# Performance work log

Measured on AMD Instinct MI355X. Metric: run time of the kernel, lower is better.

Reference implementation:

```python
import jax, jax.numpy as jnp
import numpy as np

D, H, KVH, HD, FF = 768, 12, 4, 64, 2048
N_REP = H // KVH
EPS = 1e-6


def rmsnorm(x, w):
    # Faithful to source: norm = ||x|| * n^{-1/2}; eps added to norm (not inside sqrt)
    norm = jnp.sqrt(jnp.sum(x * x, axis=-1, keepdims=True)) * (x.shape[-1] ** -0.5)
    return w * x / (norm + EPS)


def rope_tables(seq_len, head_dim, base=10000.0):
    inv_freq = 1.0 / (base ** (np.arange(0, head_dim, 2, dtype=np.float32) / head_dim))
    t = np.arange(seq_len, dtype=np.float32)
    freqs = np.einsum('i,j->ij', t, inv_freq)  # [S, HD/2]
    emb = np.concatenate([freqs, freqs], axis=-1)  # [S, HD]
    return jnp.asarray(np.cos(emb)), jnp.asarray(np.sin(emb))


def rotate_half(x):
    h = x.shape[-1] // 2
    return jnp.concatenate([-x[..., h:], x[..., :h]], axis=-1)


def setup_inputs() -> dict:
    key = jax.random.key(0)
    ks = jax.random.split(key, 9)
    s = 0.02
    return {
        'x': jax.random.normal(ks[0], (2, 2048, D), jnp.float32),
        'Wq': jax.random.normal(ks[1], (H * HD, D), jnp.float32) * s,
        'Wk': jax.random.normal(ks[2], (KVH * HD, D), jnp.float32) * s,
        'Wv': jax.random.normal(ks[3], (KVH * HD, D), jnp.float32) * s,
        'Wo': jax.random.normal(ks[4], (D, H * HD), jnp.float32) * s,
        'Wgate': jax.random.normal(ks[5], (FF, D), jnp.float32) * s,
        'Wup': jax.random.normal(ks[6], (FF, D), jnp.float32) * s,
        'Wdown': jax.random.normal(ks[7], (D, FF), jnp.float32) * s,
        'g1': jnp.ones((D,), jnp.float32),
        'g2': jnp.ones((D,), jnp.float32),
    }


def reference(x, Wq, Wk, Wv, Wo, Wgate, Wup, Wdown, g1, g2):
    B, S, _ = x.shape
    # ---- attention sublayer (pre-norm) ----
    xn = rmsnorm(x, g1)
    q = (xn @ Wq.T).reshape(B, S, H, HD).transpose(0, 2, 1, 3)      # [B,H,S,HD]
    k = (xn @ Wk.T).reshape(B, S, KVH, HD).transpose(0, 2, 1, 3)    # [B,KVH,S,HD]
    v = (xn @ Wv.T).reshape(B, S, KVH, HD).transpose(0, 2, 1, 3)
    cos, sin = rope_tables(S, HD)                                   # [S,HD]
    q = q * cos + rotate_half(q) * sin
    k = k * cos + rotate_half(k) * sin
    # repeat kv heads to match q heads
    k = jnp.repeat(k, N_REP, axis=1)                                # [B,H,S,HD]
    v = jnp.repeat(v, N_REP, axis=1)
    scores = jnp.einsum('bhqd,bhkd->bhqk', q, k) / jnp.sqrt(jnp.float32(HD))
    causal = jnp.tril(jnp.ones((S, S), bool))
    scores = jnp.where(causal, scores, jnp.finfo(scores.dtype).min)
    attn = jax.nn.softmax(scores, axis=-1)
    out = jnp.einsum('bhqk,bhkd->bhqd', attn, v)                    # [B,H,S,HD]
    out = out.transpose(0, 2, 1, 3).reshape(B, S, H * HD) @ Wo.T
    x = x + out
    # ---- SwiGLU FFN sublayer (pre-norm) ----
    xn2 = rmsnorm(x, g2)
    ff = (jax.nn.silu(xn2 @ Wgate.T) * (xn2 @ Wup.T)) @ Wdown.T
    return x + ff
```

## Files before the change

### kernel.cpp

```cpp
#include <hip/hip_runtime.h>
#include <hip/hip_bf16.h>
#include <math.h>

typedef __bf16 bf16;
typedef __attribute__((ext_vector_type(8))) __bf16 bf16x8;
typedef __attribute__((ext_vector_type(4))) __bf16 bf16x4;
typedef __attribute__((ext_vector_type(4))) float f32x4;

#define MFMA16(a,b,c) __builtin_amdgcn_mfma_f32_16x16x32_bf16(a,b,c,0,0,0)

#define BATCH 2
#define SEQ   2048
#define DMODEL 768
#define NH    12
#define NKV   4
#define NREP  3
#define HD    64
#define FFDIM 2048
#define ROWS  (BATCH*SEQ)

#define QSCALE 0.18033688011112042f
#define LOG2E  1.4426950408889634f

__device__ __forceinline__ void gl2lds16(const bf16* g, bf16* l) {
  __builtin_amdgcn_global_load_lds(
      (const __attribute__((address_space(1))) void*)g,
      (__attribute__((address_space(3))) void*)l, 16, 0, 0);
}

__device__ __forceinline__ bf16x8 pack8(f32x4 a, f32x4 b) {
  bf16x8 o;
  o[0] = (bf16)a[0]; o[1] = (bf16)a[1]; o[2] = (bf16)a[2]; o[3] = (bf16)a[3];
  o[4] = (bf16)b[0]; o[5] = (bf16)b[1]; o[6] = (bf16)b[2]; o[7] = (bf16)b[3];
  return o;
}

__global__ __launch_bounds__(256) void rope_tab_kernel(float* __restrict__ tab) {
  int id = blockIdx.x * 256 + threadIdx.x;
  int j = id >> 11, s = id & 2047;
  float inv = expf(-(float)j * (9.210340371976184f / 32.0f));
  float ang = (float)s * inv;
  tab[id] = cosf(ang);
  tab[65536 + id] = sinf(ang);
}

__global__ __launch_bounds__(256) void rmsnorm_kernel(const float* __restrict__ x,
    const float* __restrict__ g, bf16* __restrict__ out) {
  int row = blockIdx.x;
  const float* xr = x + (size_t)row * DMODEL;
  int t = threadIdx.x;
  float v0 = xr[t], v1 = xr[t + 256], v2 = xr[t + 512];
  float ss = v0 * v0 + v1 * v1 + v2 * v2;
  #pragma unroll
  for (int off = 32; off; off >>= 1) ss += __shfl_xor(ss, off, 64);
  __shared__ float red[4];
  if ((t & 63) == 0) red[t >> 6] = ss;
  __syncthreads();
  float total = red[0] + red[1] + red[2] + red[3];
  float norm = sqrtf(total) * 0.03608439182435161f;
  float sc = 1.0f / (norm + 1e-6f);
  bf16* orow = out + (size_t)row * DMODEL;
  orow[t]       = (bf16)(g[t]       * v0 * sc);
  orow[t + 256] = (bf16)(g[t + 256] * v1 * sc);
  orow[t + 512] = (bf16)(g[t + 512] * v2 * sc);
}

template<bool RES, typename OUTT>
__global__ __launch_bounds__(256) void gemm_bt64f_kernel(const bf16* __restrict__ A,
    const float* __restrict__ Bf, OUTT* __restrict__ C, const float* __restrict__ R,
    int N, int K) {
  __shared__ __align__(16) bf16 At[64 * 32];
  __shared__ __align__(16) bf16 Bt[128 * 32];
  int t = threadIdx.x;
  int lane = t & 63;
  int wave = t >> 6;
  int l15 = lane & 15, lq = lane >> 4;
  int wrow = (wave >> 1) * 32, wcol = (wave & 1) * 64;
  int row0 = blockIdx.y * 64;
  int col0 = blockIdx.x * 128;
  int srow = t >> 2, sseg = (t & 3) * 8;
  const bf16* Ag0 = A + (size_t)(row0 + srow) * K + sseg;
  const float* Bg0 = Bf + (size_t)(col0 + srow) * K + sseg;
  const float* Bg1 = Bg0 + (size_t)64 * K;
  bf16* Al0 = At + t * 8;
  bf16* Bl0 = Bt + t * 8;
  bf16* Bl1 = Bt + 2048 + t * 8;

  f32x4 b0a = *(const f32x4*)(Bg0), b0b = *(const f32x4*)(Bg0 + 4);
  f32x4 b1a = *(const f32x4*)(Bg1), b1b = *(const f32x4*)(Bg1 + 4);

  f32x4 zero = {0.f, 0.f, 0.f, 0.f};
  f32x4 acc[2][4];
  #pragma unroll
  for (int m = 0; m < 2; ++m)
    #pragma unroll
    for (int n = 0; n < 4; ++n) acc[m][n] = zero;

  for (int k0 = 0; k0 < K; k0 += 32) {
    __syncthreads();
    gl2lds16(Ag0 + k0, Al0);
    *(bf16x8*)Bl0 = pack8(b0a, b0b);
    *(bf16x8*)Bl1 = pack8(b1a, b1b);
    if (k0 + 32 < K) {
      b0a = *(const f32x4*)(Bg0 + k0 + 32); b0b = *(const f32x4*)(Bg0 + k0 + 36);
      b1a = *(const f32x4*)(Bg1 + k0 + 32); b1b = *(const f32x4*)(Bg1 + k0 + 36);
    }
    __syncthreads();
    bf16x8 af[2], bfr[4];
    #pragma unroll
    for (int m = 0; m < 2; ++m)
      af[m] = *(const bf16x8*)(At + (wrow + m * 16 + l15) * 32 + lq * 8);
    #pragma unroll
    for (int n = 0; n < 4; ++n)
      bfr[n] = *(const bf16x8*)(Bt + (wcol + n * 16 + l15) * 32 + lq * 8);
    #pragma unroll
    for (int m = 0; m < 2; ++m)
      #pragma unroll
      for (int n = 0; n < 4; ++n)
        acc[m][n] = MFMA16(af[m], bfr[n], acc[m][n]);
  }
  #pragma unroll
  for (int m = 0; m < 2; ++m)
    #pragma unroll
    for (int n = 0; n < 4; ++n)
      #pragma unroll
      for (int r = 0; r < 4; ++r) {
        size_t idx = (size_t)(row0 + wrow + m * 16 + lq * 4 + r) * N
                   + (col0 + wcol + n * 16 + l15);
        float v = acc[m][n][r];
        if (RES) v += R[idx];
        C[idx] = (OUTT)v;
      }
}

__global__ __launch_bounds__(256) void gemm_qkv_kernel(const bf16* __restrict__ A,
    const float* __restrict__ Wq, const float* __restrict__ Wk, const float* __restrict__ Wv,
    const float* __restrict__ tab, bf16* __restrict__ Qh, bf16* __restrict__ Kh,
    bf16* __restrict__ Vt) {
  __shared__ __align__(16) bf16 At[64 * 32];
  __shared__ __align__(16) bf16 Bt[128 * 32];
  const int K = DMODEL;
  int t = threadIdx.x;
  int lane = t & 63, wave = t >> 6;
  int l15 = lane & 15, lq = lane >> 4;
  int wrow = (wave >> 1) * 32, wcol = (wave & 1) * 64;
  int row0 = blockIdx.y * 64;
  int col0 = blockIdx.x * 128;
  int srow = t >> 2, sseg = (t & 3) * 8;

  const float* Bsrc; int brow;
  if (col0 < 768)       { Bsrc = Wq; brow = col0; }
  else if (col0 < 1024) { Bsrc = Wk; brow = col0 - 768; }
  else                  { Bsrc = Wv; brow = col0 - 1024; }

  const bf16* Ag0 = A + (size_t)(row0 + srow) * K + sseg;
  const float* Bg0 = Bsrc + (size_t)(brow + srow) * K + sseg;
  const float* Bg1 = Bg0 + (size_t)64 * K;
  bf16* Al0 = At + t * 8;
  bf16* Bl0 = Bt + t * 8;
  bf16* Bl1 = Bt + 2048 + t * 8;

  f32x4 b0a = *(const f32x4*)(Bg0), b0b = *(const f32x4*)(Bg0 + 4);
  f32x4 b1a = *(const f32x4*)(Bg1), b1b = *(const f32x4*)(Bg1 + 4);

  f32x4 zero = {0.f, 0.f, 0.f, 0.f};
  f32x4 acc[2][4];
  #pragma unroll
  for (int m = 0; m < 2; ++m)
    #pragma unroll
    for (int n = 0; n < 4; ++n) acc[m][n] = zero;

  for (int k0 = 0; k0 < K; k0 += 32) {
    __syncthreads();
    gl2lds16(Ag0 + k0, Al0);
    *(bf16x8*)Bl0 = pack8(b0a, b0b);
    *(bf16x8*)Bl1 = pack8(b1a, b1b);
    if (k0 + 32 < K) {
      b0a = *(const f32x4*)(Bg0 + k0 + 32); b0b = *(const f32x4*)(Bg0 + k0 + 36);
      b1a = *(const f32x4*)(Bg1 + k0 + 32); b1b = *(const f32x4*)(Bg1 + k0 + 36);
    }
    __syncthreads();
    bf16x8 af[2], bfr[4];
    #pragma unroll
    for (int m = 0; m < 2; ++m)
      af[m] = *(const bf16x8*)(At + (wrow + m * 16 + l15) * 32 + lq * 8);
    #pragma unroll
    for (int n = 0; n < 4; ++n)
      bfr[n] = *(const bf16x8*)(Bt + (wcol + n * 16 + l15) * 32 + lq * 8);
    #pragma unroll
    for (int m = 0; m < 2; ++m)
      #pragma unroll
      for (int n = 0; n < 4; ++n)
        acc[m][n] = MFMA16(af[m], bfr[n], acc[m][n]);
  }

  int b = row0 >> 11;
  int s0 = (row0 & 2047) + wrow + lq * 4;
  int colw = col0 + wcol;
  if (colw < 768) {
    int h = colw >> 6;
    f32x4 cv[2][2], sv[2][2];
    #pragma unroll
    for (int m = 0; m < 2; ++m)
      #pragma unroll
      for (int jh = 0; jh < 2; ++jh) {
        const float* cp = tab + (jh * 16 + l15) * 2048 + s0 + m * 16;
        cv[m][jh] = *(const f32x4*)cp;
        sv[m][jh] = *(const f32x4*)(cp + 65536);
      }
    #pragma unroll
    for (int m = 0; m < 2; ++m)
      #pragma unroll
      for (int n = 0; n < 4; ++n) {
        float sgn = (n < 2) ? -1.f : 1.f;
        #pragma unroll
        for (int r = 0; r < 4; ++r) {
          float c = cv[m][n & 1][r], si = sv[m][n & 1][r];
          float rp = (acc[m][n][r] * c + sgn * acc[m][n ^ 2][r] * si) * QSCALE;
          Qh[((size_t)(b * NH + h) * SEQ + s0 + m * 16 + r) * 64 + n * 16 + l15] = (bf16)rp;
        }
      }
  } else if (colw < 1024) {
    int kh = (colw - 768) >> 6;
    f32x4 cv[2][2], sv[2][2];
    #pragma unroll
    for (int m = 0; m < 2; ++m)
      #pragma unroll
      for (int jh = 0; jh < 2; ++jh) {
        const float* cp = tab + (jh * 16 + l15) * 2048 + s0 + m * 16;
        cv[m][jh] = *(const f32x4*)cp;
        sv[m][jh] = *(const f32x4*)(cp + 65536);
      }
    #pragma unroll
    for (int m = 0; m < 2; ++m)
      #pragma unroll
      for (int n = 0; n < 4; ++n) {
        float sgn = (n < 2) ? -1.f : 1.f;
        #pragma unroll
        for (int r = 0; r < 4; ++r) {
          float c = cv[m][n & 1][r], si = sv[m][n & 1][r];
          float rp = acc[m][n][r] * c + sgn * acc[m][n ^ 2][r] * si;
          Kh[((size_t)(b * NKV + kh) * SEQ + s0 + m * 16 + r) * 64 + n * 16 + l15] = (bf16)rp;
        }
      }
  } else {
    int vh = (colw - 1024) >> 6;
    #pragma unroll
    for (int m = 0; m < 2; ++m)
      #pragma unroll
      for (int n = 0; n < 4; ++n) {
        bf16x4 pv;
        #pragma unroll
        for (int r = 0; r < 4; ++r) pv[r] = (bf16)acc[m][n][r];
        *(bf16x4*)(Vt + ((size_t)(b * NKV + vh) * 64 + n * 16 + l15) * SEQ + s0 + m * 16) = pv;
      }
  }
}

__global__ __launch_bounds__(256) void gemm_gu_kernel(const bf16* __restrict__ A,
    const float* __restrict__ Wg, const float* __restrict__ Wu, bf16* __restrict__ H) {
  __shared__ __align__(16) bf16 At[128 * 32];
  __shared__ __align__(16) bf16 Bgt[64 * 32];
  __shared__ __align__(16) bf16 But[64 * 32];
  const int K = DMODEL;
  int t = threadIdx.x;
  int lane = t & 63, wave = t >> 6;
  int l15 = lane & 15, lq = lane >> 4;
  int wrow = (wave >> 1) * 64, wcol = (wave & 1) * 32;
  int row0 = blockIdx.y * 128;
  int col0 = blockIdx.x * 64;
  int srow = t >> 2, sseg = (t & 3) * 8;
  const bf16* Ag0 = A + (size_t)(row0 + srow) * K + sseg;
  const bf16* Ag1 = Ag0 + (size_t)64 * K;
  const float* Gg = Wg + (size_t)(col0 + srow) * K + sseg;
  const float* Ug = Wu + (size_t)(col0 + srow) * K + sseg;
  bf16* Al0 = At + t * 8;
  bf16* Al1 = At + 2048 + t * 8;
  bf16* Bgd = Bgt + t * 8;
  bf16* Bud = But + t * 8;

  f32x4 ga = *(const f32x4*)(Gg), gb = *(const f32x4*)(Gg + 4);
  f32x4 ua = *(const f32x4*)(Ug), ub = *(const f32x4*)(Ug + 4);

  f32x4 zero = {0.f, 0.f, 0.f, 0.f};
  f32x4 ag[4][2], au[4][2];
  #pragma unroll
  for (int m = 0; m < 4; ++m)
    #pragma unroll
    for (int n = 0; n < 2; ++n) { ag[m][n] = zero; au[m][n] = zero; }

  for (int k0 = 0; k0 < K; k0 += 32) {
    __syncthreads();
    gl2lds16(Ag0 + k0, Al0);
    gl2lds16(Ag1 + k0, Al1);
    *(bf16x8*)Bgd = pack8(ga, gb);
    *(bf16x8*)Bud = pack8(ua, ub);
    if (k0 + 32 < K) {
      ga = *(const f32x4*)(Gg + k0 + 32); gb = *(const f32x4*)(Gg + k0 + 36);
      ua = *(const f32x4*)(Ug + k0 + 32); ub = *(const f32x4*)(Ug + k0 + 36);
    }
    __syncthreads();
    bf16x8 af[4], bg[2], bu[2];
    #pragma unroll
    for (int m = 0; m < 4; ++m)
      af[m] = *(const bf16x8*)(At + (wrow + m * 16 + l15) * 32 + lq * 8);
    #pragma unroll
    for (int n = 0; n < 2; ++n) {
      bg[n] = *(const bf16x8*)(Bgt + (wcol + n * 16 + l15) * 32 + lq * 8);
      bu[n] = *(const bf16x8*)(But + (wcol + n * 16 + l15) * 32 + lq * 8);
    }
    #pragma unroll
    for (int m = 0; m < 4; ++m)
      #pragma unroll
      for (int n = 0; n < 2; ++n) {
        ag[m][n] = MFMA16(af[m], bg[n], ag[m][n]);
        au[m][n] = MFMA16(af[m], bu[n], au[m][n]);
      }
  }
  #pragma unroll
  for (int m = 0; m < 4; ++m)
    #pragma unroll
    for (int n = 0; n < 2; ++n)
      #pragma unroll
      for (int r = 0; r < 4; ++r) {
        int row = row0 + wrow + m * 16 + lq * 4 + r;
        int col = col0 + wcol + n * 16 + l15;
        float g = ag[m][n][r], u = au[m][n][r];
        float sg = g / (1.f + __builtin_amdgcn_exp2f(-g * LOG2E));
        H[(size_t)row * FFDIM + col] = (bf16)(sg * u);
      }
}

__global__ __launch_bounds__(256) void attn_kernel(const bf16* __restrict__ Qh,
    const bf16* __restrict__ Kh, const bf16* __restrict__ Vt, bf16* __restrict__ out) {
  __shared__ __align__(16) bf16 Kl0[64 * 32];
  __shared__ __align__(16) bf16 Kl1[64 * 32];
  __shared__ __align__(16) bf16 Vl0[64 * 32];
  __shared__ __align__(16) bf16 Vl1[64 * 32];
  __shared__ __align__(16) bf16 P[4][16 * 80];

  int idx = blockIdx.x;
  int qt = 31 - (idx / 24);
  int bh = idx % 24;
  int q0blk = qt * 64;
  int b = bh / NH, h = bh % NH;
  int kvh = h / NREP;
  int t = threadIdx.x;
  int lane = t & 63, wave = t >> 6;
  int l15 = lane & 15, lq = lane >> 4;
  int qw = q0blk + wave * 16;
  const bf16* Qb = Qh + (size_t)(b * NH + h) * SEQ * 64;
  const bf16* Kb = Kh + (size_t)(b * NKV + kvh) * SEQ * 64;
  const bf16* Vb = Vt + (size_t)(b * NKV + kvh) * 64 * SEQ;

  bf16x8 bq0 = *(const bf16x8*)(Qb + (size_t)(qw + l15) * 64 + lq * 8);
  bf16x8 bq1 = *(const bf16x8*)(Qb + (size_t)(qw + l15) * 64 + 32 + lq * 8);

  const bf16* Kg = Kb + (size_t)(t >> 2) * 64 + (t & 3) * 8;
  const bf16* Vg = Vb + (size_t)(t >> 2) * SEQ + (t & 3) * 8;
  bf16* Kl0d = Kl0 + t * 8;
  bf16* Kl1d = Kl1 + t * 8;
  bf16* Vl0d = Vl0 + t * 8;
  bf16* Vl1d = Vl1 + t * 8;
  bf16* Pw = P[wave];
  int Pwq = l15 * 80, lq8 = lq * 8, lq4 = lq * 4;

  f32x4 zero = {0.f, 0.f, 0.f, 0.f};
  f32x4 o[4];
  o[0] = zero; o[1] = zero; o[2] = zero; o[3] = zero;
  float l_r = 0.f;

  for (int k0 = 0; k0 <= q0blk + 63; k0 += 64) {
    __syncthreads();
    gl2lds16(Kg + (size_t)k0 * 64, Kl0d);
    gl2lds16(Kg + (size_t)k0 * 64 + 32, Kl1d);
    gl2lds16(Vg + k0, Vl0d);
    gl2lds16(Vg + k0 + 32, Vl1d);
    __syncthreads();
    f32x4 s[4];
    #pragma unroll
    for (int c = 0; c < 4; ++c) {
      bf16x8 ak0 = *(const bf16x8*)(Kl0 + (c * 16 + l15) * 32 + lq8);
      bf16x8 ak1 = *(const bf16x8*)(Kl1 + (c * 16 + l15) * 32 + lq8);
      s[c] = zero;
      s[c] = MFMA16(ak0, bq0, s[c]);
      s[c] = MFMA16(ak1, bq1, s[c]);
    }
    if (k0 + 63 > qw) {
      int qmk = qw + l15 - k0 - lq4;
      #pragma unroll
      for (int c = 0; c < 4; ++c)
        #pragma unroll
        for (int r = 0; r < 4; ++r)
          if (c * 16 + r > qmk) s[c][r] = -INFINITY;
    }
    #pragma unroll
    for (int c = 0; c < 4; ++c) {
      bf16x4 pe;
      #pragma unroll
      for (int r = 0; r < 4; ++r) {
        float e = __builtin_amdgcn_exp2f(s[c][r]);
        l_r += e;
        pe[r] = (bf16)e;
      }
      *(bf16x4*)(Pw + Pwq + c * 16 + lq4) = pe;
    }
    bf16x8 bp0 = *(const bf16x8*)(Pw + Pwq + lq8);
    bf16x8 bp1 = *(const bf16x8*)(Pw + Pwq + 32 + lq8);
    #pragma unroll
    for (int n = 0; n < 4; ++n) {
      bf16x8 av0 = *(const bf16x8*)(Vl0 + (n * 16 + l15) * 32 + lq8);
      bf16x8 av1 = *(const bf16x8*)(Vl1 + (n * 16 + l15) * 32 + lq8);
      o[n] = MFMA16(av0, bp0, o[n]);
      o[n] = MFMA16(av1, bp1, o[n]);
    }
  }
  float lt = l_r;
  lt += __shfl_xor(lt, 16, 64);
  lt += __shfl_xor(lt, 32, 64);
  float inv = 1.f / lt;
  int q = qw + l15;
  bf16* orow = out + (size_t)(b * SEQ + q) * DMODEL + h * 64;
  #pragma unroll
  for (int n = 0; n < 4; ++n) {
    bf16x4 po;
    #pragma unroll
    for (int r = 0; r < 4; ++r) po[r] = (bf16)(o[n][r] * inv);
    *(bf16x4*)(orow + n * 16 + lq4) = po;
  }
}

extern "C" void kernel_launch(void* const* d_in, const int* in_sizes, int n_in,
                              void* d_out, int out_size, void* d_ws, size_t ws_size,
                              hipStream_t stream) {
  const float* x     = (const float*)d_in[0];
  const float* Wq    = (const float*)d_in[1];
  const float* Wk    = (const float*)d_in[2];
  const float* Wv    = (const float*)d_in[3];
  const float* Wo    = (const float*)d_in[4];
  const float* Wgate = (const float*)d_in[5];
  const float* Wup   = (const float*)d_in[6];
  const float* Wdown = (const float*)d_in[7];
  const float* g1    = (const float*)d_in[8];
  const float* g2    = (const float*)d_in[9];
  float* out = (float*)d_out;

  char* ws = (char*)d_ws;
  size_t off = 0;
  auto alloc = [&](size_t bytes) { size_t o = off; off += (bytes + 255) & ~(size_t)255; return o; };
  size_t o_tab = alloc((size_t)2 * 32 * 2048 * 4);
  size_t o_x1  = alloc((size_t)4096 * 768 * 4);
  size_t o_H   = alloc((size_t)4096 * 2048 * 2);
  size_t o_xn  = alloc((size_t)4096 * 768 * 2);
  size_t o_Qh  = alloc((size_t)2 * 12 * 2048 * 64 * 2);
  size_t o_Kh  = alloc((size_t)2 * 4 * 2048 * 64 * 2);
  size_t o_Vt  = alloc((size_t)2 * 4 * 64 * 2048 * 2);
  size_t o_ao  = alloc((size_t)4096 * 768 * 2);
  if (ws_size < off) return;

  float* tab  = (float*)(ws + o_tab);
  float* fx1  = (float*)(ws + o_x1);
  bf16* bH    = (bf16*)(ws + o_H);
  bf16* bxn   = (bf16*)(ws + o_xn);
  bf16* bQh   = (bf16*)(ws + o_Qh);
  bf16* bKh   = (bf16*)(ws + o_Kh);
  bf16* bVt   = (bf16*)(ws + o_Vt);
  bf16* bao   = (bf16*)(ws + o_ao);

  rope_tab_kernel<<<256, 256, 0, stream>>>(tab);

  rmsnorm_kernel<<<4096, 256, 0, stream>>>(x, g1, bxn);
  gemm_qkv_kernel<<<dim3(10, 64), 256, 0, stream>>>(bxn, Wq, Wk, Wv, tab, bQh, bKh, bVt);
  attn_kernel<<<dim3(768), 256, 0, stream>>>(bQh, bKh, bVt, bao);
  gemm_bt64f_kernel<true, float><<<dim3(6, 64), 256, 0, stream>>>(bao, Wo, fx1, x, 768, 768);

  rmsnorm_kernel<<<4096, 256, 0, stream>>>(fx1, g2, bxn);
  gemm_gu_kernel<<<dim3(32, 32), 256, 0, stream>>>(bxn, Wgate, Wup, bH);
  gemm_bt64f_kernel<true, float><<<dim3(6, 64), 256, 0, stream>>>(bH, Wdown, out, fx1, 768, 2048);
}
```

Measured before the change: 268.3 us.

## Split-K the Wo and Wdown GEMMs with separate residual reduce; vectorize rmsnorm

The Wo and Wdown projections now run as split-K GEMMs (2 and 4 chunks) that write fp32 partials, followed by a reduce kernel that sums the partials and adds the residual. The goal is to fill more of the GPU, since the original 384-block grids leave many CUs idle. RMSNorm now uses 192 threads with float4 loads and bf16x4 stores. The workspace is reorganized into a shared arena that aliases the attention buffers with the FFN hidden buffer and the partials. The cost is extra global traffic for the partials and two additional kernel launches.

```diff
diff --git a/kernel.cpp b/kernel.cpp
--- a/kernel.cpp
+++ b/kernel.cpp
@@ -44,31 +44,30 @@
   tab[65536 + id] = sinf(ang);
 }
 
-__global__ __launch_bounds__(256) void rmsnorm_kernel(const float* __restrict__ x,
+__global__ __launch_bounds__(192) void rmsnorm_kernel(const float* __restrict__ x,
     const float* __restrict__ g, bf16* __restrict__ out) {
   int row = blockIdx.x;
   const float* xr = x + (size_t)row * DMODEL;
   int t = threadIdx.x;
-  float v0 = xr[t], v1 = xr[t + 256], v2 = xr[t + 512];
-  float ss = v0 * v0 + v1 * v1 + v2 * v2;
+  f32x4 v = *(const f32x4*)(xr + t * 4);
+  float ss = v[0] * v[0] + v[1] * v[1] + v[2] * v[2] + v[3] * v[3];
   #pragma unroll
   for (int off = 32; off; off >>= 1) ss += __shfl_xor(ss, off, 64);
-  __shared__ float red[4];
+  __shared__ float red[3];
   if ((t & 63) == 0) red[t >> 6] = ss;
   __syncthreads();
-  float total = red[0] + red[1] + red[2] + red[3];
+  float total = red[0] + red[1] + red[2];
   float norm = sqrtf(total) * 0.03608439182435161f;
   float sc = 1.0f / (norm + 1e-6f);
-  bf16* orow = out + (size_t)row * DMODEL;
-  orow[t]       = (bf16)(g[t]       * v0 * sc);
-  orow[t + 256] = (bf16)(g[t + 256] * v1 * sc);
-  orow[t + 512] = (bf16)(g[t + 512] * v2 * sc);
-}
-
-template<bool RES, typename OUTT>
-__global__ __launch_bounds__(256) void gemm_bt64f_kernel(const bf16* __restrict__ A,
-    const float* __restrict__ Bf, OUTT* __restrict__ C, const float* __restrict__ R,
-    int N, int K) {
+  f32x4 gv = *(const f32x4*)(g + t * 4);
+  bf16x4 o;
+  #pragma unroll
+  for (int i = 0; i < 4; ++i) o[i] = (bf16)(gv[i] * v[i] * sc);
+  *(bf16x4*)(out + (size_t)row * DMODEL + t * 4) = o;
+}
+
+__global__ __launch_bounds__(256) void gemm_split_kernel(const bf16* __restrict__ A,
+    const float* __restrict__ Bf, float* __restrict__ P, int N, int Ktot, int KCHUNK) {
   __shared__ __align__(16) bf16 At[64 * 32];
   __shared__ __align__(16) bf16 Bt[128 * 32];
   int t = threadIdx.x;
@@ -78,10 +77,13 @@
   int wrow = (wave >> 1) * 32, wcol = (wave & 1) * 64;
   int row0 = blockIdx.y * 64;
   int col0 = blockIdx.x * 128;
+  int s = blockIdx.z;
+  int kbeg = s * KCHUNK;
+  int klen = KCHUNK;
   int srow = t >> 2, sseg = (t & 3) * 8;
-  const bf16* Ag0 = A + (size_t)(row0 + srow) * K + sseg;
-  const float* Bg0 = Bf + (size_t)(col0 + srow) * K + sseg;
-  const float* Bg1 = Bg0 + (size_t)64 * K;
+  const bf16* Ag0 = A + (size_t)(row0 + srow) * Ktot + kbeg + sseg;
+  const float* Bg0 = Bf + (size_t)(col0 + srow) * Ktot + kbeg + sseg;
+  const float* Bg1 = Bg0 + (size_t)64 * Ktot;
   bf16* Al0 = At + t * 8;
   bf16* Bl0 = Bt + t * 8;
   bf16* Bl1 = Bt + 2048 + t * 8;
@@ -96,12 +98,12 @@
     #pragma unroll
     for (int n = 0; n < 4; ++n) acc[m][n] = zero;
 
-  for (int k0 = 0; k0 < K; k0 += 32) {
+  for (int k0 = 0; k0 < klen; k0 += 32) {
     __syncthreads();
     gl2lds16(Ag0 + k0, Al0);
     *(bf16x8*)Bl0 = pack8(b0a, b0b);
     *(bf16x8*)Bl1 = pack8(b1a, b1b);
-    if (k0 + 32 < K) {
+    if (k0 + 32 < klen) {
       b0a = *(const f32x4*)(Bg0 + k0 + 32); b0b = *(const f32x4*)(Bg0 + k0 + 36);
       b1a = *(const f32x4*)(Bg1 + k0 + 32); b1b = *(const f32x4*)(Bg1 + k0 + 36);
     }
@@ -119,6 +121,7 @@
       for (int n = 0; n < 4; ++n)
         acc[m][n] = MFMA16(af[m], bfr[n], acc[m][n]);
   }
+  float* Ps = P + (size_t)s * ROWS * N;
   #pragma unroll
   for (int m = 0; m < 2; ++m)
     #pragma unroll
@@ -127,10 +130,19 @@
       for (int r = 0; r < 4; ++r) {
         size_t idx = (size_t)(row0 + wrow + m * 16 + lq * 4 + r) * N
                    + (col0 + wcol + n * 16 + l15);
-        float v = acc[m][n][r];
-        if (RES) v += R[idx];
-        C[idx] = (OUTT)v;
-      }
+        Ps[idx] = acc[m][n][r];
+      }
+}
+
+template<int S>
+__global__ __launch_bounds__(256) void reduce_kernel(const float* __restrict__ P,
+    const float* __restrict__ R, float* __restrict__ O) {
+  const size_t stride4 = (size_t)ROWS * DMODEL / 4;
+  size_t i = (size_t)blockIdx.x * 256 + threadIdx.x;
+  f32x4 acc = ((const f32x4*)R)[i];
+  #pragma unroll
+  for (int s = 0; s < S; ++s) acc += ((const f32x4*)P)[s * stride4 + i];
+  ((f32x4*)O)[i] = acc;
 }
 
 __global__ __launch_bounds__(256) void gemm_qkv_kernel(const bf16* __restrict__ A,
@@ -450,31 +462,38 @@
   auto alloc = [&](size_t bytes) { size_t o = off; off += (bytes + 255) & ~(size_t)255; return o; };
   size_t o_tab = alloc((size_t)2 * 32 * 2048 * 4);
   size_t o_x1  = alloc((size_t)4096 * 768 * 4);
-  size_t o_H   = alloc((size_t)4096 * 2048 * 2);
   size_t o_xn  = alloc((size_t)4096 * 768 * 2);
-  size_t o_Qh  = alloc((size_t)2 * 12 * 2048 * 64 * 2);
-  size_t o_Kh  = alloc((size_t)2 * 4 * 2048 * 64 * 2);
-  size_t o_Vt  = alloc((size_t)2 * 4 * 64 * 2048 * 2);
-  size_t o_ao  = alloc((size_t)4096 * 768 * 2);
+  size_t arena = alloc((size_t)67108864);
+  size_t o_Qh  = arena;
+  size_t o_Kh  = o_Qh + (size_t)6291456;
+  size_t o_Vt  = o_Kh + (size_t)2097152;
+  size_t o_ao  = o_Vt + (size_t)2097152;
+  size_t o_Pwo = arena + (size_t)16777216;
+  size_t o_H   = arena;
+  size_t o_Pdn = arena + (size_t)16777216;
   if (ws_size < off) return;
 
   float* tab  = (float*)(ws + o_tab);
   float* fx1  = (float*)(ws + o_x1);
-  bf16* bH    = (bf16*)(ws + o_H);
   bf16* bxn   = (bf16*)(ws + o_xn);
   bf16* bQh   = (bf16*)(ws + o_Qh);
   bf16* bKh   = (bf16*)(ws + o_Kh);
   bf16* bVt   = (bf16*)(ws + o_Vt);
   bf16* bao   = (bf16*)(ws + o_ao);
+  float* Pwo  = (float*)(ws + o_Pwo);
+  bf16* bH    = (bf16*)(ws + o_H);
+  float* Pdn  = (float*)(ws + o_Pdn);
 
   rope_tab_kernel<<<256, 256, 0, stream>>>(tab);
 
-  rmsnorm_kernel<<<4096, 256, 0, stream>>>(x, g1, bxn);
+  rmsnorm_kernel<<<4096, 192, 0, stream>>>(x, g1, bxn);
   gemm_qkv_kernel<<<dim3(10, 64), 256, 0, stream>>>(bxn, Wq, Wk, Wv, tab, bQh, bKh, bVt);
   attn_kernel<<<dim3(768), 256, 0, stream>>>(bQh, bKh, bVt, bao);
-  gemm_bt64f_kernel<true, float><<<dim3(6, 64), 256, 0, stream>>>(bao, Wo, fx1, x, 768, 768);
-
-  rmsnorm_kernel<<<4096, 256, 0, stream>>>(fx1, g2, bxn);
+  gemm_split_kernel<<<dim3(6, 64, 2), 256, 0, stream>>>(bao, Wo, Pwo, 768, 768, 384);
+  reduce_kernel<2><<<3072, 256, 0, stream>>>(Pwo, x, fx1);
+
+  rmsnorm_kernel<<<4096, 192, 0, stream>>>(fx1, g2, bxn);
   gemm_gu_kernel<<<dim3(32, 32), 256, 0, stream>>>(bxn, Wgate, Wup, bH);
-  gemm_bt64f_kernel<true, float><<<dim3(6, 64), 256, 0, stream>>>(bH, Wdown, out, fx1, 768, 2048);
-}
+  gemm_split_kernel<<<dim3(6, 64, 4), 256, 0, stream>>>(bH, Wdown, Pdn, 768, 2048, 512);
+  reduce_kernel<4><<<3072, 256, 0, stream>>>(Pdn, fx1, out);
+}
```

Result: slower. 275.1 us (+2.5%).

## Replace LDS-staged output GEMMs with register-direct loads; vectorize RMSNorm

Applied to the files above, without the earlier changes.

The Wo and Wdown projection GEMMs now load A and B fragments straight from global memory into registers, with two-stage software prefetching. This removes shared-memory staging and block-wide barriers. Each wave computes its own 32x64 tile, and the grid is reshaped to 128x64 block tiles. Because waves no longer share operands through LDS, the same weight data is reloaded more often from global memory and cache. RMSNorm is also rewritten to use 192 threads with float4 loads and bf16x4 stores, and the workspace allocation order is shuffled.

```diff
diff --git a/kernel.cpp b/kernel.cpp
--- a/kernel.cpp
+++ b/kernel.cpp
@@ -44,50 +44,63 @@
   tab[65536 + id] = sinf(ang);
 }
 
-__global__ __launch_bounds__(256) void rmsnorm_kernel(const float* __restrict__ x,
+__global__ __launch_bounds__(192) void rmsnorm_kernel(const float* __restrict__ x,
     const float* __restrict__ g, bf16* __restrict__ out) {
   int row = blockIdx.x;
   const float* xr = x + (size_t)row * DMODEL;
   int t = threadIdx.x;
-  float v0 = xr[t], v1 = xr[t + 256], v2 = xr[t + 512];
-  float ss = v0 * v0 + v1 * v1 + v2 * v2;
+  f32x4 v = *(const f32x4*)(xr + t * 4);
+  float ss = v[0] * v[0] + v[1] * v[1] + v[2] * v[2] + v[3] * v[3];
   #pragma unroll
   for (int off = 32; off; off >>= 1) ss += __shfl_xor(ss, off, 64);
-  __shared__ float red[4];
+  __shared__ float red[3];
   if ((t & 63) == 0) red[t >> 6] = ss;
   __syncthreads();
-  float total = red[0] + red[1] + red[2] + red[3];
+  float total = red[0] + red[1] + red[2];
   float norm = sqrtf(total) * 0.03608439182435161f;
   float sc = 1.0f / (norm + 1e-6f);
-  bf16* orow = out + (size_t)row * DMODEL;
-  orow[t]       = (bf16)(g[t]       * v0 * sc);
-  orow[t + 256] = (bf16)(g[t + 256] * v1 * sc);
-  orow[t + 512] = (bf16)(g[t + 512] * v2 * sc);
-}
-
-template<bool RES, typename OUTT>
-__global__ __launch_bounds__(256) void gemm_bt64f_kernel(const bf16* __restrict__ A,
-    const float* __restrict__ Bf, OUTT* __restrict__ C, const float* __restrict__ R,
+  f32x4 gv = *(const f32x4*)(g + t * 4);
+  bf16x4 o;
+  #pragma unroll
+  for (int i = 0; i < 4; ++i) o[i] = (bf16)(gv[i] * v[i] * sc);
+  *(bf16x4*)(out + (size_t)row * DMODEL + t * 4) = o;
+}
+
+struct BStage { f32x4 v[8]; };
+
+__device__ __forceinline__ void loadB(const float* Bbase, int k, BStage& s, int K) {
+  #pragma unroll
+  for (int n = 0; n < 4; ++n) {
+    const float* p = Bbase + (size_t)(n * 16) * K + k;
+    s.v[n * 2]     = *(const f32x4*)(p);
+    s.v[n * 2 + 1] = *(const f32x4*)(p + 4);
+  }
+}
+
+__device__ __forceinline__ void loadA(const bf16* Abase, int k, bf16x8& a0, bf16x8& a1, int K) {
+  a0 = *(const bf16x8*)(Abase + k);
+  a1 = *(const bf16x8*)(Abase + (size_t)16 * K + k);
+}
+
+__device__ __forceinline__ void gstep(f32x4 acc[2][4], bf16x8 a0, bf16x8 a1, const BStage& s) {
+  #pragma unroll
+  for (int n = 0; n < 4; ++n) {
+    bf16x8 bb = pack8(s.v[2 * n], s.v[2 * n + 1]);
+    acc[0][n] = MFMA16(a0, bb, acc[0][n]);
+    acc[1][n] = MFMA16(a1, bb, acc[1][n]);
+  }
+}
+
+__global__ __launch_bounds__(256) void gemm_reg_kernel(const bf16* __restrict__ A,
+    const float* __restrict__ Bf, float* __restrict__ C, const float* __restrict__ R,
     int N, int K) {
-  __shared__ __align__(16) bf16 At[64 * 32];
-  __shared__ __align__(16) bf16 Bt[128 * 32];
   int t = threadIdx.x;
-  int lane = t & 63;
-  int wave = t >> 6;
+  int lane = t & 63, wave = t >> 6;
   int l15 = lane & 15, lq = lane >> 4;
-  int wrow = (wave >> 1) * 32, wcol = (wave & 1) * 64;
-  int row0 = blockIdx.y * 64;
-  int col0 = blockIdx.x * 128;
-  int srow = t >> 2, sseg = (t & 3) * 8;
-  const bf16* Ag0 = A + (size_t)(row0 + srow) * K + sseg;
-  const float* Bg0 = Bf + (size_t)(col0 + srow) * K + sseg;
-  const float* Bg1 = Bg0 + (size_t)64 * K;
-  bf16* Al0 = At + t * 8;
-  bf16* Bl0 = Bt + t * 8;
-  bf16* Bl1 = Bt + 2048 + t * 8;
-
-  f32x4 b0a = *(const f32x4*)(Bg0), b0b = *(const f32x4*)(Bg0 + 4);
-  f32x4 b1a = *(const f32x4*)(Bg1), b1b = *(const f32x4*)(Bg1 + 4);
+  int row0 = blockIdx.y * 128 + wave * 32;
+  int col0 = blockIdx.x * 64;
+  const bf16* Abase = A + (size_t)(row0 + l15) * K + lq * 8;
+  const float* Bbase = Bf + (size_t)(col0 + l15) * K + lq * 8;
 
   f32x4 zero = {0.f, 0.f, 0.f, 0.f};
   f32x4 acc[2][4];
@@ -96,40 +109,28 @@
     #pragma unroll
     for (int n = 0; n < 4; ++n) acc[m][n] = zero;
 
-  for (int k0 = 0; k0 < K; k0 += 32) {
-    __syncthreads();
-    gl2lds16(Ag0 + k0, Al0);
-    *(bf16x8*)Bl0 = pack8(b0a, b0b);
-    *(bf16x8*)Bl1 = pack8(b1a, b1b);
-    if (k0 + 32 < K) {
-      b0a = *(const f32x4*)(Bg0 + k0 + 32); b0b = *(const f32x4*)(Bg0 + k0 + 36);
-      b1a = *(const f32x4*)(Bg1 + k0 + 32); b1b = *(const f32x4*)(Bg1 + k0 + 36);
-    }
-    __syncthreads();
-    bf16x8 af[2], bfr[4];
-    #pragma unroll
-    for (int m = 0; m < 2; ++m)
-      af[m] = *(const bf16x8*)(At + (wrow + m * 16 + l15) * 32 + lq * 8);
+  bf16x8 a0A, a1A, a0B, a1B;
+  BStage bA, bB;
+  loadA(Abase, 0, a0A, a1A, K);  loadB(Bbase, 0, bA, K);
+  loadA(Abase, 32, a0B, a1B, K); loadB(Bbase, 32, bB, K);
+
+  for (int k0 = 0; k0 < K; k0 += 64) {
+    int kA = (k0 + 64 < K) ? k0 + 64 : 0;
+    int kB = (k0 + 96 < K) ? k0 + 96 : 0;
+    gstep(acc, a0A, a1A, bA);
+    loadA(Abase, kA, a0A, a1A, K); loadB(Bbase, kA, bA, K);
+    gstep(acc, a0B, a1B, bB);
+    loadA(Abase, kB, a0B, a1B, K); loadB(Bbase, kB, bB, K);
+  }
+
+  #pragma unroll
+  for (int m = 0; m < 2; ++m)
     #pragma unroll
     for (int n = 0; n < 4; ++n)
-      bfr[n] = *(const bf16x8*)(Bt + (wcol + n * 16 + l15) * 32 + lq * 8);
-    #pragma unroll
-    for (int m = 0; m < 2; ++m)
-      #pragma unroll
-      for (int n = 0; n < 4; ++n)
-        acc[m][n] = MFMA16(af[m], bfr[n], acc[m][n]);
-  }
-  #pragma unroll
-  for (int m = 0; m < 2; ++m)
-    #pragma unroll
-    for (int n = 0; n < 4; ++n)
       #pragma unroll
       for (int r = 0; r < 4; ++r) {
-        size_t idx = (size_t)(row0 + wrow + m * 16 + lq * 4 + r) * N
-                   + (col0 + wcol + n * 16 + l15);
-        float v = acc[m][n][r];
-        if (RES) v += R[idx];
-        C[idx] = (OUTT)v;
+        size_t idx = (size_t)(row0 + m * 16 + lq * 4 + r) * N + (col0 + n * 16 + l15);
+        C[idx] = acc[m][n][r] + R[idx];
       }
 }
 
@@ -450,31 +451,31 @@
   auto alloc = [&](size_t bytes) { size_t o = off; off += (bytes + 255) & ~(size_t)255; return o; };
   size_t o_tab = alloc((size_t)2 * 32 * 2048 * 4);
   size_t o_x1  = alloc((size_t)4096 * 768 * 4);
-  size_t o_H   = alloc((size_t)4096 * 2048 * 2);
   size_t o_xn  = alloc((size_t)4096 * 768 * 2);
   size_t o_Qh  = alloc((size_t)2 * 12 * 2048 * 64 * 2);
   size_t o_Kh  = alloc((size_t)2 * 4 * 2048 * 64 * 2);
   size_t o_Vt  = alloc((size_t)2 * 4 * 64 * 2048 * 2);
   size_t o_ao  = alloc((size_t)4096 * 768 * 2);
+  size_t o_H   = alloc((size_t)4096 * 2048 * 2);
   if (ws_size < off) return;
 
   float* tab  = (float*)(ws + o_tab);
   float* fx1  = (float*)(ws + o_x1);
-  bf16* bH    = (bf16*)(ws + o_H);
   bf16* bxn   = (bf16*)(ws + o_xn);
   bf16* bQh   = (bf16*)(ws + o_Qh);
   bf16* bKh   = (bf16*)(ws + o_Kh);
   bf16* bVt   = (bf16*)(ws + o_Vt);
   bf16* bao   = (bf16*)(ws + o_ao);
+  bf16* bH    = (bf16*)(ws + o_H);
 
   rope_tab_kernel<<<256, 256, 0, stream>>>(tab);
 
-  rmsnorm_kernel<<<4096, 256, 0, stream>>>(x, g1, bxn);
+  rmsnorm_kernel<<<4096, 192, 0, stream>>>(x, g1, bxn);
   gemm_qkv_kernel<<<dim3(10, 64), 256, 0, stream>>>(bxn, Wq, Wk, Wv, tab, bQh, bKh, bVt);
   attn_kernel<<<dim3(768), 256, 0, stream>>>(bQh, bKh, bVt, bao);
-  gemm_bt64f_kernel<true, float><<<dim3(6, 64), 256, 0, stream>>>(bao, Wo, fx1, x, 768, 768);
-
-  rmsnorm_kernel<<<4096, 256, 0, stream>>>(fx1, g2, bxn);
+  gemm_reg_kernel<<<dim3(12, 32), 256, 0, stream>>>(bao, Wo, fx1, x, 768, 768);
+
+  rmsnorm_kernel<<<4096, 192, 0, stream>>>(fx1, g2, bxn);
   gemm_gu_kernel<<<dim3(32, 32), 256, 0, stream>>>(bxn, Wgate, Wup, bH);
-  gemm_bt64f_kernel<true, float><<<dim3(6, 64), 256, 0, stream>>>(bH, Wdown, out, fx1, 768, 2048);
-}
+  gemm_reg_kernel<<<dim3(12, 32), 256, 0, stream>>>(bH, Wdown, out, fx1, 768, 2048);
+}
```

Measured after the change: 398.7 us. +48.6%, slower.
